# Kernel tuning notes

Hardware: AMD Instinct MI355X
Metric: run time of the kernel (lower is better)

The kernel has to match this reference:

```python
import jax, jax.numpy as jnp
import numpy as np

B, S, HID = 2, 2048, 2048
NH, NOPE, ROPE = 16, 128, 64
HD = NOPE + ROPE          # 192
VHD = 128
KVR, QR = 512, 1536
FFN = 5632
THETA = 10000.0
EPS = 1e-6


def rmsnorm(x, w, eps=EPS):
    xf = x.astype(jnp.float32)
    rms = jnp.sqrt(jnp.mean(xf * xf, axis=-1, keepdims=True) + eps)
    return (xf / rms).astype(x.dtype) * w


def apply_rope(x, cos, sin):
    # x: (..., rope_dim); half-split rotation convention
    half = x.shape[-1] // 2
    x1, x2 = x[..., :half], x[..., half:]
    return jnp.concatenate([x1 * cos - x2 * sin, x2 * cos + x1 * sin], axis=-1)


def rope_tables(seq_len, dim, theta=THETA):
    inv_freq = 1.0 / (theta ** (jnp.arange(0, dim, 2, dtype=jnp.float32) / dim))
    t = jnp.arange(seq_len, dtype=jnp.float32)
    freqs = jnp.outer(t, inv_freq)           # (S, dim/2)
    return jnp.cos(freqs), jnp.sin(freqs)


def setup_inputs():
    key = jax.random.key(0)
    ks = jax.random.split(key, 10)
    def w(k, shape, fan_in):
        return jax.random.normal(k, shape, dtype=jnp.float32) * (fan_in ** -0.5)
    return {
        'x': jax.random.normal(ks[0], (B, S, HID), dtype=jnp.float32),
        'attn_norm_w': jnp.ones((HID,), jnp.float32),
        'wq_down': w(ks[1], (HID, QR), HID),
        'wq_up': w(ks[2], (QR, NH * HD), QR),
        'wkv_down': w(ks[3], (HID, KVR + ROPE), HID),
        'kv_norm_w': jnp.ones((KVR,), jnp.float32),
        'wkv_up': w(ks[4], (KVR, NH * (NOPE + VHD)), KVR),
        'wout': w(ks[5], (NH * VHD, HID), NH * VHD),
        'ffn_norm_w': jnp.ones((HID,), jnp.float32),
        'w_gate': w(ks[6], (HID, FFN), HID),
        'w_up': w(ks[7], (HID, FFN), HID),
        'w_down': w(ks[8], (FFN, HID), FFN),
    }


def reference(x, attn_norm_w, wq_down, wq_up, wkv_down, kv_norm_w, wkv_up, wout,
              ffn_norm_w, w_gate, w_up, w_down):
    scale = 1.0 / np.sqrt(HD)
    # --- attention sub-block ---
    h = rmsnorm(x, attn_norm_w)
    q = (h @ wq_down) @ wq_up                       # (B,S,NH*HD)
    q = q.reshape(B, S, NH, HD)
    q_nope, q_rope = q[..., :NOPE], q[..., NOPE:]
    kv_full = h @ wkv_down                          # (B,S,KVR+ROPE)
    kv_c, k_rope = kv_full[..., :KVR], kv_full[..., KVR:]
    kv_c = rmsnorm(kv_c, kv_norm_w)
    kv_exp = (kv_c @ wkv_up).reshape(B, S, NH, NOPE + VHD)
    k_nope, v = kv_exp[..., :NOPE], kv_exp[..., NOPE:]

    cos, sin = rope_tables(S, ROPE)                 # (S, ROPE/2)
    cos4, sin4 = cos[None, :, None, :], sin[None, :, None, :]
    q_rope = apply_rope(q_rope, cos4, sin4)         # (B,S,NH,ROPE)
    k_rope = apply_rope(k_rope[:, :, None, :], cos4, sin4)  # (B,S,1,ROPE)
    k_rope = jnp.broadcast_to(k_rope, (B, S, NH, ROPE))

    q_full = jnp.concatenate([q_nope, q_rope], axis=-1)     # (B,S,NH,HD)
    k = jnp.concatenate([k_nope, k_rope], axis=-1)          # (B,S,NH,HD)

    scores = jnp.einsum('bqhd,bkhd->bhqk', q_full, k) * scale
    causal = jnp.tril(jnp.ones((S, S), dtype=bool))
    scores = jnp.where(causal[None, None], scores, jnp.finfo(scores.dtype).min)
    probs = jax.nn.softmax(scores, axis=-1)
    attn = jnp.einsum('bhqk,bkhd->bqhd', probs, v).reshape(B, S, NH * VHD)
    x = x + attn @ wout

    # --- SwiGLU MLP sub-block ---
    h2 = rmsnorm(x, ffn_norm_w)
    ffn = (jax.nn.silu(h2 @ w_gate) * (h2 @ w_up)) @ w_down
    return x + ffn
```

## Files before the change

### kernel.cpp

```cpp
#include <hip/hip_runtime.h>
#include <hip/hip_bf16.h>


using bf16x8 = __attribute__((ext_vector_type(8))) short;
using f32x4  = __attribute__((ext_vector_type(4))) float;

#define GLOBAL_AS __attribute__((address_space(1)))
#define LDS_AS    __attribute__((address_space(3)))
#define MFMA16(a, b, c) __builtin_amdgcn_mfma_f32_16x16x32_bf16((a), (b), (c), 0, 0, 0)

static constexpr int Sc = 2048;

__device__ __forceinline__ void gload16(const void* g, void* l) {
  __builtin_amdgcn_global_load_lds((const GLOBAL_AS unsigned int*)g,
                                   (LDS_AS unsigned int*)l, 16, 0, 0);
}
__device__ __forceinline__ float bf2f(unsigned short u) {
  union { float f; unsigned int i; } x; x.i = ((unsigned int)u) << 16; return x.f;
}
__device__ __forceinline__ unsigned short f2bf(float f) {
  union { float f; unsigned int i; } x; x.f = f;
  unsigned int i = x.i;
  return (unsigned short)((i + 0x7fffu + ((i >> 16) & 1u)) >> 16);
}
__device__ __forceinline__ int swz4(int r) { return ((r >> 2) & 3) ^ (r & 3); }

__global__ void fill_k(float* out, float v, int n) {
  int i = blockIdx.x * 256 + threadIdx.x;
  if (i < n) out[i] = v;
}

__global__ __launch_bounds__(256) void wtrans(const float* __restrict__ W,
                                              unsigned short* __restrict__ WT,
                                              int K, int N) {
  __shared__ float t[32][33];
  const int n0 = blockIdx.x * 32, k0 = blockIdx.y * 32;
  const int tx = threadIdx.x & 31, ty = threadIdx.x >> 5;
#pragma unroll
  for (int i = 0; i < 4; ++i) {
    int k = k0 + ty + i * 8;
    int n = n0 + tx;
    t[ty + i * 8][tx] = (n < N) ? W[(size_t)k * N + n] : 0.0f;
  }
  __syncthreads();
#pragma unroll
  for (int i = 0; i < 4; ++i) {
    int n = n0 + ty + i * 8;
    int k = k0 + tx;
    WT[(size_t)n * K + k] = f2bf(t[tx][ty + i * 8]);
  }
}

__global__ void rope_tab(float* __restrict__ cosT, float* __restrict__ sinT) {
  int i = blockIdx.x * 256 + threadIdx.x;
  if (i >= Sc * 32) return;
  int s = i >> 5, j = i & 31;
  float inv = powf(10000.0f, -(float)j / 32.0f);
  float a = (float)s * inv;
  cosT[i] = cosf(a);
  sinT[i] = sinf(a);
}

__global__ __launch_bounds__(256) void rmsnorm_k(const float* __restrict__ in,
                                                 const float* __restrict__ w,
                                                 unsigned short* __restrict__ out,
                                                 int D, int istride, int ostride) {
  const int row = blockIdx.x;
  const float* x = in + (size_t)row * istride;
  float ss = 0.f;
  for (int c = threadIdx.x * 4; c < D; c += 1024) {
    const float4 v = *(const float4*)(x + c);
    ss += v.x * v.x + v.y * v.y + v.z * v.z + v.w * v.w;
  }
#pragma unroll
  for (int off = 1; off < 64; off <<= 1) ss += __shfl_xor(ss, off);
  __shared__ float part[4];
  if ((threadIdx.x & 63) == 0) part[threadIdx.x >> 6] = ss;
  __syncthreads();
  float tot = part[0] + part[1] + part[2] + part[3];
  float r = rsqrtf(tot / (float)D + 1e-6f);
  for (int c = threadIdx.x * 4; c < D; c += 1024) {
    const float4 v = *(const float4*)(x + c);
    ushort4 o;
    o.x = f2bf(v.x * r * w[c + 0]);
    o.y = f2bf(v.y * r * w[c + 1]);
    o.z = f2bf(v.z * r * w[c + 2]);
    o.w = f2bf(v.w * r * w[c + 3]);
    *(ushort4*)(out + (size_t)row * ostride + c) = o;
  }
}

enum { EPI_BF16 = 0, EPI_F32 = 1, EPI_ADDF32 = 2, EPI_SILU = 3 };

template <int EPI>
__global__ __launch_bounds__(256) void gemm_bt(const unsigned short* __restrict__ A,
                                               const unsigned short* __restrict__ BT,
                                               void* __restrict__ Cp,
                                               const float* __restrict__ resid,
                                               const unsigned short* __restrict__ other,
                                               int M, int N, int K) {
  __shared__ unsigned short ldsA[2][128 * 32];
  __shared__ unsigned short ldsB[2][128 * 32];
  const int tid = threadIdx.x;
  const int w = tid >> 6, lane = tid & 63;

  const int nwg = gridDim.x;
  const int orig = blockIdx.x;
  const int qq = nwg >> 3, rr = nwg & 7;
  const int xcd = orig & 7, lidx = orig >> 3;
  const int fswz = (xcd < rr ? xcd * (qq + 1) : rr * (qq + 1) + (xcd - rr) * qq) + lidx;
  const int m0 = (fswz & 31) * 128;
  const int n0 = (fswz >> 5) * 128;

  const int wm = (w >> 1) * 64, wn = (w & 1) * 64;
  const int rl = lane & 15, gsel = lane >> 4;

  const int p0 = w * 64 + lane;
  const int p1 = p0 + 256;
  const int r0 = p0 >> 2, r1 = p1 >> 2;
  const int g0 = (p0 & 3) ^ swz4(r0), g1 = (p1 & 3) ^ swz4(r1);
  const unsigned short* gA0 = A + (size_t)(m0 + r0) * K + g0 * 8;
  const unsigned short* gA1 = A + (size_t)(m0 + r1) * K + g1 * 8;
  const unsigned short* gB0 = BT + (size_t)(n0 + r0) * K + g0 * 8;
  const unsigned short* gB1 = BT + (size_t)(n0 + r1) * K + g1 * 8;
  const int dA0 = (w * 64) * 8, dA1 = dA0 + 2048;

  int aoff[4], boff[4];
#pragma unroll
  for (int i = 0; i < 4; ++i) {
    int ra = wm + i * 16 + rl;
    aoff[i] = ra * 32 + (gsel ^ swz4(ra)) * 8;
    int rb = wn + i * 16 + rl;
    boff[i] = rb * 32 + (gsel ^ swz4(rb)) * 8;
  }

  auto STAGE = [&](int kt, int p) {
    const int ko = kt * 32;
    gload16(gA0 + ko, &ldsA[p][dA0]);
    gload16(gA1 + ko, &ldsA[p][dA1]);
    gload16(gB0 + ko, &ldsB[p][dA0]);
    gload16(gB1 + ko, &ldsB[p][dA1]);
  };

  f32x4 acc[4][4] = {};
  const int nk = K >> 5;

  STAGE(0, 0);
  STAGE(1, 1);
  for (int kt = 0; kt < nk; ++kt) {
    asm volatile("s_waitcnt vmcnt(4)" ::: "memory");
    __builtin_amdgcn_s_barrier();
    __builtin_amdgcn_sched_barrier(0);
    const unsigned short* lA = &ldsA[kt & 1][0];
    const unsigned short* lB = &ldsB[kt & 1][0];
    bf16x8 a[4], b[4];
#pragma unroll
    for (int i = 0; i < 4; ++i) a[i] = *(const bf16x8*)&lA[aoff[i]];
#pragma unroll
    for (int i = 0; i < 4; ++i) b[i] = *(const bf16x8*)&lB[boff[i]];
    __builtin_amdgcn_s_setprio(1);
#pragma unroll
    for (int i = 0; i < 4; ++i)
#pragma unroll
      for (int j = 0; j < 4; ++j) acc[i][j] = MFMA16(a[i], b[j], acc[i][j]);
    __builtin_amdgcn_s_setprio(0);
    __builtin_amdgcn_sched_barrier(0);
    __builtin_amdgcn_s_barrier();
    const int nxt = (kt + 2 < nk) ? kt + 2 : nk - 1;
    STAGE(nxt, kt & 1);
  }

#pragma unroll
  for (int i = 0; i < 4; ++i) {
#pragma unroll
    for (int j = 0; j < 4; ++j) {
#pragma unroll
      for (int rg = 0; rg < 4; ++rg) {
        const int row = m0 + wm + i * 16 + gsel * 4 + rg;
        const int col = n0 + wn + j * 16 + rl;
        const size_t idx = (size_t)row * N + col;
        const float v = acc[i][j][rg];
        if constexpr (EPI == EPI_BF16) {
          ((unsigned short*)Cp)[idx] = f2bf(v);
        } else if constexpr (EPI == EPI_F32) {
          ((float*)Cp)[idx] = v;
        } else if constexpr (EPI == EPI_ADDF32) {
          ((float*)Cp)[idx] = v + resid[idx];
        } else {
          float gv = bf2f(other[idx]);
          float sg = gv / (1.f + __expf(-gv));
          ((unsigned short*)Cp)[idx] = f2bf(sg * v);
        }
      }
    }
  }
}

__global__ __launch_bounds__(256) void repack_q(const unsigned short* __restrict__ q,
                                                const float* __restrict__ cosT,
                                                const float* __restrict__ sinT,
                                                unsigned short* __restrict__ Qc) {
  const int row = blockIdx.x;
  const int b = row >> 11, s = row & 2047;
  const float scale = 0.07216878364870322f;
  const unsigned short* qr = q + (size_t)row * 3072;
  for (int i = threadIdx.x; i < 3072; i += 256) {
    int h = i / 192, d = i - h * 192;
    float v;
    if (d < 128) {
      v = bf2f(qr[h * 192 + d]);
    } else {
      int j = d - 128;
      int jj = j & 31;
      float x1 = bf2f(qr[h * 192 + 128 + jj]);
      float x2 = bf2f(qr[h * 192 + 160 + jj]);
      float c = cosT[s * 32 + jj], sn = sinT[s * 32 + jj];
      v = (j < 32) ? (x1 * c - x2 * sn) : (x2 * c + x1 * sn);
    }
    Qc[((size_t)(b * 16 + h) * Sc + s) * 192 + d] = f2bf(v * scale);
  }
}

__global__ __launch_bounds__(256) void repack_kv(const unsigned short* __restrict__ kvex,
                                                 const float* __restrict__ kvf,
                                                 const float* __restrict__ cosT,
                                                 const float* __restrict__ sinT,
                                                 unsigned short* __restrict__ Kc,
                                                 unsigned short* __restrict__ VT) {
  __shared__ unsigned short vt_lds[32][136];
  const int bid = blockIdx.x;
  const int st = bid & 63;
  const int h = (bid >> 6) & 15;
  const int b = bid >> 10;
  const int s0 = st * 32;
  const int tid = threadIdx.x;
  const size_t KcBase = (size_t)(b * 16 + h) * Sc;
  for (int i = tid; i < 32 * 32; i += 256) {
    int r = i >> 5, g = i & 31;
    uint4 vdat = *(const uint4*)(kvex + (size_t)(b * Sc + s0 + r) * 4096 + h * 256 + g * 8);
    if (g < 16) {
      *(uint4*)(Kc + (KcBase + s0 + r) * 192 + g * 8) = vdat;
    } else {
      *(uint4*)(&vt_lds[r][(g - 16) * 8]) = vdat;
    }
  }
  for (int i = tid; i < 32 * 64; i += 256) {
    int r = i >> 6, d = i & 63;
    int s = s0 + r;
    int jj = d & 31;
    const float* kvrow = kvf + (size_t)(b * Sc + s) * 640;
    float x1 = kvrow[512 + jj], x2 = kvrow[544 + jj];
    float c = cosT[s * 32 + jj], sn = sinT[s * 32 + jj];
    float v = (d < 32) ? (x1 * c - x2 * sn) : (x2 * c + x1 * sn);
    Kc[(KcBase + s) * 192 + 128 + d] = f2bf(v);
  }
  __syncthreads();
  const int f = tid >> 1, sh = (tid & 1) * 16;
  unsigned int vals[8];
#pragma unroll
  for (int k2 = 0; k2 < 8; ++k2) {
    unsigned int lo = vt_lds[sh + 2 * k2][f];
    unsigned int hi = vt_lds[sh + 2 * k2 + 1][f];
    vals[k2] = lo | (hi << 16);
  }
  unsigned short* dst = VT + ((size_t)(b * 16 + h) * 128 + f) * Sc + s0 + sh;
  ((uint4*)dst)[0] = make_uint4(vals[0], vals[1], vals[2], vals[3]);
  ((uint4*)dst)[1] = make_uint4(vals[4], vals[5], vals[6], vals[7]);
}

__global__ __launch_bounds__(256) void attn_k(const unsigned short* __restrict__ Qc,
                                              const unsigned short* __restrict__ Kc,
                                              const unsigned short* __restrict__ VT,
                                              unsigned short* __restrict__ Ob) {
  __shared__ unsigned short lds_k[2][32 * 192];
  __shared__ unsigned short lds_v[2][128 * 32];
  __shared__ __align__(16) unsigned short p_lds[4][16 * 40];
  const int tid = threadIdx.x, w = tid >> 6, lane = tid & 63;
  const int rl = lane & 15, gh = lane >> 4;
  const int bidx = blockIdx.x;
  const int bh = bidx & 31;
  const int qt = 31 - (bidx >> 5);
  const unsigned short* Qh = Qc + (size_t)bh * Sc * 192;
  const unsigned short* Kh = Kc + (size_t)bh * Sc * 192;
  const unsigned short* Vh = VT + (size_t)bh * 128 * Sc;
  const int qr0 = qt * 64 + w * 16;

  bf16x8 qf[6];
#pragma unroll
  for (int kk = 0; kk < 6; ++kk)
    qf[kk] = *(const bf16x8*)(Qh + (size_t)(qr0 + rl) * 192 + kk * 32 + gh * 8);

  f32x4 o[8] = {};
  float mrun[4] = {-1e30f, -1e30f, -1e30f, -1e30f};
  float srun[4] = {0.f, 0.f, 0.f, 0.f};

  int kr[3], kg[3];
#pragma unroll
  for (int j = 0; j < 3; ++j) {
    int pp = j * 256 + w * 64 + lane;
    int r = pp / 24, gq = pp - r * 24;
    kr[j] = r;
    kg[j] = (gq & ~7) | ((gq & 7) ^ (r & 7));
  }
  int vr[2], vg[2];
#pragma unroll
  for (int j = 0; j < 2; ++j) {
    int pp = j * 256 + w * 64 + lane;
    int r = pp >> 2;
    vr[j] = r;
    vg[j] = (pp & 3) ^ swz4(r);
  }

  auto STAGE = [&](int t, int b) {
    const int k0 = t * 32;
#pragma unroll
    for (int j = 0; j < 3; ++j)
      gload16(Kh + (size_t)(k0 + kr[j]) * 192 + kg[j] * 8,
              &lds_k[b][(j * 256 + w * 64) * 8]);
#pragma unroll
    for (int j = 0; j < 2; ++j)
      gload16(Vh + (size_t)vr[j] * Sc + k0 + vg[j] * 8,
              &lds_v[b][(j * 256 + w * 64) * 8]);
  };

  STAGE(0, 0);
  asm volatile("s_waitcnt vmcnt(0)" ::: "memory");
  __builtin_amdgcn_s_barrier();
  __builtin_amdgcn_sched_barrier(0);

  const int nt = 2 * qt + 2;
  int cur = 0;
  for (int t = 0; t < nt; ++t) {
    if (t + 1 < nt) STAGE(t + 1, cur ^ 1);
    const int k0 = t * 32;
    if (k0 <= qr0 + 15) {
      const unsigned short* lk = lds_k[cur];
      const unsigned short* lv = lds_v[cur];
      f32x4 s0 = {0.f, 0.f, 0.f, 0.f}, s1 = {0.f, 0.f, 0.f, 0.f};
      __builtin_amdgcn_s_setprio(1);
#pragma unroll
      for (int kk = 0; kk < 6; ++kk) {
        const int gq = kk * 4 + gh;
        const int ph0 = (gq & ~7) | ((gq & 7) ^ (rl & 7));
        bf16x8 kf0 = *(const bf16x8*)&lk[rl * 192 + ph0 * 8];
        s0 = MFMA16(qf[kk], kf0, s0);
        bf16x8 kf1 = *(const bf16x8*)&lk[(16 + rl) * 192 + ph0 * 8];
        s1 = MFMA16(qf[kk], kf1, s1);
      }
      __builtin_amdgcn_s_setprio(0);
      if (k0 + 31 > qr0) {
#pragma unroll
        for (int rg = 0; rg < 4; ++rg) {
          int qrow = qr0 + gh * 4 + rg;
          if (k0 + rl > qrow) s0[rg] = -1e30f;
          if (k0 + 16 + rl > qrow) s1[rg] = -1e30f;
        }
      }
      float al[4];
#pragma unroll
      for (int rg = 0; rg < 4; ++rg) {
        float v = fmaxf(s0[rg], s1[rg]);
        v = fmaxf(v, __shfl_xor(v, 1));
        v = fmaxf(v, __shfl_xor(v, 2));
        v = fmaxf(v, __shfl_xor(v, 4));
        v = fmaxf(v, __shfl_xor(v, 8));
        float mn = fmaxf(mrun[rg], v);
        al[rg] = __expf(mrun[rg] - mn);
        mrun[rg] = mn;
        float p0 = __expf(s0[rg] - mn), p1 = __expf(s1[rg] - mn);
        s0[rg] = p0;
        s1[rg] = p1;
        float rs = p0 + p1;
        rs += __shfl_xor(rs, 1);
        rs += __shfl_xor(rs, 2);
        rs += __shfl_xor(rs, 4);
        rs += __shfl_xor(rs, 8);
        srun[rg] = srun[rg] * al[rg] + rs;
      }
#pragma unroll
      for (int i = 0; i < 8; ++i)
#pragma unroll
        for (int rg = 0; rg < 4; ++rg) o[i][rg] *= al[rg];
      unsigned short* pw = p_lds[w];
#pragma unroll
      for (int rg = 0; rg < 4; ++rg) {
        pw[(gh * 4 + rg) * 40 + rl] = f2bf(s0[rg]);
        pw[(gh * 4 + rg) * 40 + 16 + rl] = f2bf(s1[rg]);
      }
      bf16x8 pa = *(const bf16x8*)&pw[rl * 40 + gh * 8];
      __builtin_amdgcn_s_setprio(1);
#pragma unroll
      for (int vf = 0; vf < 8; ++vf) {
        int r = vf * 16 + rl;
        bf16x8 vfr = *(const bf16x8*)&lv[r * 32 + (gh ^ swz4(r)) * 8];
        o[vf] = MFMA16(pa, vfr, o[vf]);
      }
      __builtin_amdgcn_s_setprio(0);
    }
    asm volatile("s_waitcnt vmcnt(0)" ::: "memory");
    __builtin_amdgcn_s_barrier();
    __builtin_amdgcn_sched_barrier(0);
    cur ^= 1;
  }
  const int b = bh >> 4, hh = bh & 15;
  float rd[4];
#pragma unroll
  for (int rg = 0; rg < 4; ++rg) rd[rg] = 1.f / srun[rg];
#pragma unroll
  for (int vf = 0; vf < 8; ++vf) {
#pragma unroll
    for (int rg = 0; rg < 4; ++rg) {
      int srow = qr0 + gh * 4 + rg;
      int col = hh * 128 + vf * 16 + rl;
      Ob[((size_t)(b * Sc) + srow) * 2048 + col] = f2bf(o[vf][rg] * rd[rg]);
    }
  }
}

extern "C" void kernel_launch(void* const* d_in, const int* in_sizes, int n_in,
                              void* d_out, int out_size, void* d_ws, size_t ws_size,
                              hipStream_t stream) {
  (void)in_sizes; (void)n_in;
  const float* x    = (const float*)d_in[0];
  const float* anw  = (const float*)d_in[1];
  const float* wqd  = (const float*)d_in[2];
  const float* wqu  = (const float*)d_in[3];
  const float* wkvd = (const float*)d_in[4];
  const float* kvnw = (const float*)d_in[5];
  const float* wkvu = (const float*)d_in[6];
  const float* wout = (const float*)d_in[7];
  const float* fnw  = (const float*)d_in[8];
  const float* wg   = (const float*)d_in[9];
  const float* wu   = (const float*)d_in[10];
  const float* wd   = (const float*)d_in[11];
  float* out = (float*)d_out;

  char* ws = (char*)d_ws;
  size_t off = 0;
  auto alloc = [&](size_t bytes) -> char* {
    char* p = ws + off;
    off += (bytes + 255) & ~(size_t)255;
    return p;
  };
  unsigned short* wslot = (unsigned short*)alloc(5632ull * 2048 * 2);
  float* cosT           = (float*)alloc(2048ull * 32 * 4);
  float* sinT           = (float*)alloc(2048ull * 32 * 4);
  unsigned short* hbuf  = (unsigned short*)alloc(4096ull * 2048 * 2);
  char* arena           = alloc(4096ull * 1536 * 2 + 4096ull * 3072 * 2);
  float* kvf            = (float*)alloc(4096ull * 640 * 4);
  unsigned short* kvn   = (unsigned short*)alloc(4096ull * 512 * 2);
  unsigned short* Qc    = (unsigned short*)alloc(32ull * 2048 * 192 * 2);
  unsigned short* Kc    = (unsigned short*)alloc(32ull * 2048 * 192 * 2);
  unsigned short* VTb   = (unsigned short*)alloc(32ull * 128 * 2048 * 2);
  const size_t NEED = off;

  if (ws_size < NEED) {
    fill_k<<<dim3((out_size + 255) / 256), dim3(256), 0, stream>>>(
        out, (float)(ws_size >> 20), out_size);
    return;
  }

  unsigned short* qd    = (unsigned short*)arena;
  unsigned short* q     = (unsigned short*)(arena + 4096ull * 1536 * 2);
  unsigned short* kvex  = (unsigned short*)arena;
  unsigned short* h     = hbuf;
  unsigned short* attnb = hbuf;
  unsigned short* h2    = hbuf;
  unsigned short* gbuf  = Qc;
  float* x2             = out;

  dim3 blk(256);
  rope_tab<<<dim3(256), blk, 0, stream>>>(cosT, sinT);
  rmsnorm_k<<<dim3(4096), blk, 0, stream>>>(x, anw, h, 2048, 2048, 2048);

  wtrans<<<dim3(48, 64), blk, 0, stream>>>(wqd, wslot, 2048, 1536);
  gemm_bt<EPI_BF16><<<dim3(12 * 32), blk, 0, stream>>>(h, wslot, qd, nullptr, nullptr, 4096, 1536, 2048);
  wtrans<<<dim3(96, 48), blk, 0, stream>>>(wqu, wslot, 1536, 3072);
  gemm_bt<EPI_BF16><<<dim3(24 * 32), blk, 0, stream>>>(qd, wslot, q, nullptr, nullptr, 4096, 3072, 1536);
  repack_q<<<dim3(4096), blk, 0, stream>>>(q, cosT, sinT, Qc);

  wtrans<<<dim3(20, 64), blk, 0, stream>>>(wkvd, wslot, 2048, 576);
  gemm_bt<EPI_F32><<<dim3(5 * 32), blk, 0, stream>>>(h, wslot, kvf, nullptr, nullptr, 4096, 640, 2048);
  rmsnorm_k<<<dim3(4096), blk, 0, stream>>>(kvf, kvnw, kvn, 512, 640, 512);
  wtrans<<<dim3(128, 16), blk, 0, stream>>>(wkvu, wslot, 512, 4096);
  gemm_bt<EPI_BF16><<<dim3(32 * 32), blk, 0, stream>>>(kvn, wslot, kvex, nullptr, nullptr, 4096, 4096, 512);
  repack_kv<<<dim3(2048), blk, 0, stream>>>(kvex, kvf, cosT, sinT, Kc, VTb);

  attn_k<<<dim3(1024), blk, 0, stream>>>(Qc, Kc, VTb, attnb);
  wtrans<<<dim3(64, 64), blk, 0, stream>>>(wout, wslot, 2048, 2048);
  gemm_bt<EPI_ADDF32><<<dim3(16 * 32), blk, 0, stream>>>(attnb, wslot, x2, x, nullptr, 4096, 2048, 2048);

  rmsnorm_k<<<dim3(4096), blk, 0, stream>>>(x2, fnw, h2, 2048, 2048, 2048);
  wtrans<<<dim3(176, 64), blk, 0, stream>>>(wg, wslot, 2048, 5632);
  gemm_bt<EPI_BF16><<<dim3(44 * 32), blk, 0, stream>>>(h2, wslot, gbuf, nullptr, nullptr, 4096, 5632, 2048);
  wtrans<<<dim3(176, 64), blk, 0, stream>>>(wu, wslot, 2048, 5632);
  gemm_bt<EPI_SILU><<<dim3(44 * 32), blk, 0, stream>>>(h2, wslot, gbuf, nullptr, gbuf, 4096, 5632, 2048);
  wtrans<<<dim3(64, 176), blk, 0, stream>>>(wd, wslot, 5632, 2048);
  gemm_bt<EPI_ADDF32><<<dim3(16 * 32), blk, 0, stream>>>(gbuf, wslot, out, x2, nullptr, 4096, 2048, 5632);
}
```

Before: 893.8 us.

## Add larger-tile 512-thread GEMM kernel for the big projections

Adds a new GEMM kernel with 512 threads, 128x256 or 256x256 output tiles, K-step 64, double-buffered direct global-to-LDS loads, XOR swizzle and s_setprio around the MFMA block. Most large projections (q down/up, kv up, output, gate/up/down) now use it instead of the 128x128 kernel. Larger tiles raise arithmetic intensity and cut global traffic per FLOP. The cost is more registers and LDS per block, fewer blocks per launch (possible tail or under-occupancy on N=1536 and 2048 shapes), and an epilogue that writes elements individually.

```diff
diff --git a/kernel.cpp b/kernel.cpp
--- a/kernel.cpp
+++ b/kernel.cpp
@@ -92,6 +92,132 @@
 
 enum { EPI_BF16 = 0, EPI_F32 = 1, EPI_ADDF32 = 2, EPI_SILU = 3 };
 
+template <int BMW, int EPI>
+__global__ __launch_bounds__(512, 2) void gemm_big(const unsigned short* __restrict__ A,
+                                                   const unsigned short* __restrict__ BT,
+                                                   void* __restrict__ Cp,
+                                                   const float* __restrict__ resid,
+                                                   const unsigned short* __restrict__ other,
+                                                   int M, int N, int K) {
+  constexpr int BM = 128 * BMW;
+  constexpr int AL = 2 * BMW;
+  constexpr int MF = 4 * BMW;
+  __shared__ unsigned short ldsA[2][BM * 64];
+  __shared__ unsigned short ldsB[2][256 * 64];
+
+  const int tid = threadIdx.x;
+  const int w = tid >> 6, lane = tid & 63;
+  const int rl = lane & 15, gh = lane >> 4;
+  const int wm = w >> 2, wn = w & 3;
+
+  const int nwg = gridDim.x;
+  const int orig = blockIdx.x;
+  const int qq = nwg >> 3, rr = nwg & 7;
+  const int xcd = orig & 7, lidx = orig >> 3;
+  const int fswz = (xcd < rr ? xcd * (qq + 1) : rr * (qq + 1) + (xcd - rr) * qq) + lidx;
+  const int MT = M / BM;
+  const int m0 = (fswz % MT) * BM;
+  const int n0 = (fswz / MT) * 256;
+
+  const unsigned short* srcA[AL];
+#pragma unroll
+  for (int i = 0; i < AL; ++i) {
+    int G = i * 512 + tid, r = G >> 3, sl = (G & 7) ^ (r & 7);
+    srcA[i] = A + (size_t)(m0 + r) * K + sl * 8;
+  }
+  const unsigned short* srcB[4];
+#pragma unroll
+  for (int i = 0; i < 4; ++i) {
+    int G = i * 512 + tid, r = G >> 3, sl = (G & 7) ^ (r & 7);
+    srcB[i] = BT + (size_t)(n0 + r) * K + sl * 8;
+  }
+
+  auto STAGE = [&](int kt, int p) {
+    const int ko = kt * 64;
+#pragma unroll
+    for (int i = 0; i < AL; ++i)
+      gload16(srcA[i] + ko, &ldsA[p][(i * 512 + w * 64) * 8]);
+#pragma unroll
+    for (int i = 0; i < 4; ++i)
+      gload16(srcB[i] + ko, &ldsB[p][(i * 512 + w * 64) * 8]);
+  };
+
+  f32x4 acc[MF][4] = {};
+  const int nk = K >> 6;
+
+  STAGE(0, 0);
+  STAGE(1, 1);
+  if constexpr (BMW == 2) asm volatile("s_waitcnt vmcnt(8)" ::: "memory");
+  else                    asm volatile("s_waitcnt vmcnt(6)" ::: "memory");
+  __builtin_amdgcn_s_barrier();
+  __builtin_amdgcn_sched_barrier(0);
+
+  for (int kt = 0; kt < nk; ++kt) {
+    const int cur = kt & 1;
+    const unsigned short* lA = &ldsA[cur][0];
+    const unsigned short* lB = &ldsB[cur][0];
+    bf16x8 a[MF][2], b[4][2];
+#pragma unroll
+    for (int mf = 0; mf < MF; ++mf)
+#pragma unroll
+      for (int ks = 0; ks < 2; ++ks) {
+        const int row = wm * (64 * BMW) + mf * 16 + rl;
+        a[mf][ks] = *(const bf16x8*)&lA[row * 64 + (((ks << 2) + gh) ^ (row & 7)) * 8];
+      }
+#pragma unroll
+    for (int nf = 0; nf < 4; ++nf)
+#pragma unroll
+      for (int ks = 0; ks < 2; ++ks) {
+        const int row = wn * 64 + nf * 16 + rl;
+        b[nf][ks] = *(const bf16x8*)&lB[row * 64 + (((ks << 2) + gh) ^ (row & 7)) * 8];
+      }
+    asm volatile("s_waitcnt lgkmcnt(0)" ::: "memory");
+    __builtin_amdgcn_sched_barrier(0);
+    __builtin_amdgcn_s_barrier();
+    __builtin_amdgcn_sched_barrier(0);
+    STAGE((kt + 2 < nk) ? kt + 2 : kt, cur);
+    __builtin_amdgcn_s_setprio(1);
+#pragma unroll
+    for (int ks = 0; ks < 2; ++ks)
+#pragma unroll
+      for (int mf = 0; mf < MF; ++mf)
+#pragma unroll
+        for (int nf = 0; nf < 4; ++nf)
+          acc[mf][nf] = MFMA16(a[mf][ks], b[nf][ks], acc[mf][nf]);
+    __builtin_amdgcn_s_setprio(0);
+    __builtin_amdgcn_sched_barrier(0);
+    if constexpr (BMW == 2) asm volatile("s_waitcnt vmcnt(8)" ::: "memory");
+    else                    asm volatile("s_waitcnt vmcnt(6)" ::: "memory");
+    __builtin_amdgcn_s_barrier();
+    __builtin_amdgcn_sched_barrier(0);
+  }
+
+#pragma unroll
+  for (int mf = 0; mf < MF; ++mf) {
+#pragma unroll
+    for (int nf = 0; nf < 4; ++nf) {
+#pragma unroll
+      for (int rg = 0; rg < 4; ++rg) {
+        const int row = m0 + wm * (64 * BMW) + mf * 16 + gh * 4 + rg;
+        const int col = n0 + wn * 64 + nf * 16 + rl;
+        const size_t idx = (size_t)row * N + col;
+        const float v = acc[mf][nf][rg];
+        if constexpr (EPI == EPI_BF16) {
+          ((unsigned short*)Cp)[idx] = f2bf(v);
+        } else if constexpr (EPI == EPI_F32) {
+          ((float*)Cp)[idx] = v;
+        } else if constexpr (EPI == EPI_ADDF32) {
+          ((float*)Cp)[idx] = v + resid[idx];
+        } else {
+          float gv = bf2f(other[idx]);
+          float sg = gv / (1.f + __expf(-gv));
+          ((unsigned short*)Cp)[idx] = f2bf(sg * v);
+        }
+      }
+    }
+  }
+}
+
 template <int EPI>
 __global__ __launch_bounds__(256) void gemm_bt(const unsigned short* __restrict__ A,
                                                const unsigned short* __restrict__ BT,
@@ -103,7 +229,6 @@
   __shared__ unsigned short ldsB[2][128 * 32];
   const int tid = threadIdx.x;
   const int w = tid >> 6, lane = tid & 63;
-
   const int nwg = gridDim.x;
   const int orig = blockIdx.x;
   const int qq = nwg >> 3, rr = nwg & 7;
@@ -469,32 +594,32 @@
   unsigned short* gbuf  = Qc;
   float* x2             = out;
 
-  dim3 blk(256);
+  dim3 blk(256), blk512(512);
   rope_tab<<<dim3(256), blk, 0, stream>>>(cosT, sinT);
   rmsnorm_k<<<dim3(4096), blk, 0, stream>>>(x, anw, h, 2048, 2048, 2048);
 
   wtrans<<<dim3(48, 64), blk, 0, stream>>>(wqd, wslot, 2048, 1536);
-  gemm_bt<EPI_BF16><<<dim3(12 * 32), blk, 0, stream>>>(h, wslot, qd, nullptr, nullptr, 4096, 1536, 2048);
+  gemm_big<1, EPI_BF16><<<dim3(32 * 6), blk512, 0, stream>>>(h, wslot, qd, nullptr, nullptr, 4096, 1536, 2048);
   wtrans<<<dim3(96, 48), blk, 0, stream>>>(wqu, wslot, 1536, 3072);
-  gemm_bt<EPI_BF16><<<dim3(24 * 32), blk, 0, stream>>>(qd, wslot, q, nullptr, nullptr, 4096, 3072, 1536);
+  gemm_big<2, EPI_BF16><<<dim3(16 * 12), blk512, 0, stream>>>(qd, wslot, q, nullptr, nullptr, 4096, 3072, 1536);
   repack_q<<<dim3(4096), blk, 0, stream>>>(q, cosT, sinT, Qc);
 
   wtrans<<<dim3(20, 64), blk, 0, stream>>>(wkvd, wslot, 2048, 576);
   gemm_bt<EPI_F32><<<dim3(5 * 32), blk, 0, stream>>>(h, wslot, kvf, nullptr, nullptr, 4096, 640, 2048);
   rmsnorm_k<<<dim3(4096), blk, 0, stream>>>(kvf, kvnw, kvn, 512, 640, 512);
   wtrans<<<dim3(128, 16), blk, 0, stream>>>(wkvu, wslot, 512, 4096);
-  gemm_bt<EPI_BF16><<<dim3(32 * 32), blk, 0, stream>>>(kvn, wslot, kvex, nullptr, nullptr, 4096, 4096, 512);
+  gemm_big<2, EPI_BF16><<<dim3(16 * 16), blk512, 0, stream>>>(kvn, wslot, kvex, nullptr, nullptr, 4096, 4096, 512);
   repack_kv<<<dim3(2048), blk, 0, stream>>>(kvex, kvf, cosT, sinT, Kc, VTb);
 
   attn_k<<<dim3(1024), blk, 0, stream>>>(Qc, Kc, VTb, attnb);
   wtrans<<<dim3(64, 64), blk, 0, stream>>>(wout, wslot, 2048, 2048);
-  gemm_bt<EPI_ADDF32><<<dim3(16 * 32), blk, 0, stream>>>(attnb, wslot, x2, x, nullptr, 4096, 2048, 2048);
+  gemm_big<1, EPI_ADDF32><<<dim3(32 * 8), blk512, 0, stream>>>(attnb, wslot, x2, x, nullptr, 4096, 2048, 2048);
 
   rmsnorm_k<<<dim3(4096), blk, 0, stream>>>(x2, fnw, h2, 2048, 2048, 2048);
   wtrans<<<dim3(176, 64), blk, 0, stream>>>(wg, wslot, 2048, 5632);
-  gemm_bt<EPI_BF16><<<dim3(44 * 32), blk, 0, stream>>>(h2, wslot, gbuf, nullptr, nullptr, 4096, 5632, 2048);
+  gemm_big<2, EPI_BF16><<<dim3(16 * 22), blk512, 0, stream>>>(h2, wslot, gbuf, nullptr, nullptr, 4096, 5632, 2048);
   wtrans<<<dim3(176, 64), blk, 0, stream>>>(wu, wslot, 2048, 5632);
-  gemm_bt<EPI_SILU><<<dim3(44 * 32), blk, 0, stream>>>(h2, wslot, gbuf, nullptr, gbuf, 4096, 5632, 2048);
+  gemm_big<2, EPI_SILU><<<dim3(16 * 22), blk512, 0, stream>>>(h2, wslot, gbuf, nullptr, gbuf, 4096, 5632, 2048);
   wtrans<<<dim3(64, 176), blk, 0, stream>>>(wd, wslot, 5632, 2048);
-  gemm_bt<EPI_ADDF32><<<dim3(16 * 32), blk, 0, stream>>>(gbuf, wslot, out, x2, nullptr, 4096, 2048, 5632);
-}
+  gemm_big<1, EPI_ADDF32><<<dim3(32 * 8), blk512, 0, stream>>>(gbuf, wslot, out, x2, nullptr, 4096, 2048, 5632);
+}
```

After: 834.0 us. 6.7% less time.
